# Optimization experiments

Measured on AMD Instinct MI355X. Metric: run time of the kernel, lower is better.

The kernel has to match this reference:

```python
import jax, jax.numpy as jnp
import numpy as np

B, N, D, H, V, E, T = 128, 49, 512, 512, 10000, 512, 20


def setup_inputs() -> dict:
    key = jax.random.key(0)
    ks = jax.random.split(key, 12)
    s = 0.02  # weight init scale
    return {
        "img_features": jax.random.normal(ks[0], (B, N, D), jnp.float32),
        "captions": jax.random.randint(ks[1], (B, T), 0, V, jnp.int32),
        "embed": jax.random.normal(ks[2], (V, E), jnp.float32) * s,
        "W_v": jax.random.normal(ks[3], (D, D), jnp.float32) * s,
        "W_h": jax.random.normal(ks[4], (D, H), jnp.float32) * s,
        "att_b": jnp.zeros((N,), jnp.float32),
        "W_a": jax.random.normal(ks[5], (D,), jnp.float32) * s,
        "W_ih": jax.random.normal(ks[6], (4 * H, E + D), jnp.float32) * s,
        "b_ih": jnp.zeros((4 * H,), jnp.float32),
        "W_hh": jax.random.normal(ks[7], (4 * H, H), jnp.float32) * s,
        "b_hh": jnp.zeros((4 * H,), jnp.float32),
        "W_out": jax.random.normal(ks[8], (V, H), jnp.float32) * s,
        "b_out": jnp.zeros((V,), jnp.float32),
    }


def reference(img_features, captions, embed, W_v, W_h, att_b, W_a,
              W_ih, b_ih, W_hh, b_hh, W_out, b_out):
    b, n, d = img_features.shape
    t_len = captions.shape[1]
    h_dim = W_hh.shape[1]
    emb = embed[captions]                       # [B,T,E]
    mean_ctx = img_features.mean(axis=1)        # [B,D] (context at t=0)
    fv = jnp.einsum('bnd,ed->bne', img_features, W_v)  # precomputed W_v @ feats

    def step(carry, xs):
        h, c = carry
        emb_t, t = xs                           # emb_t: [B,E]
        # additive attention (computed for all t; masked out at t=0)
        oh = h @ W_h.T                          # [B,D]
        act = jax.nn.relu(fv + oh[:, None, :] + att_b[None, :, None])
        a = jax.nn.softmax(act @ W_a, axis=1)   # [B,N]
        z = jnp.einsum('bnd,bn->bd', img_features, a)
        context = jnp.where(t == 0, mean_ctx, z)
        alpha = jnp.where(t == 0, jnp.zeros_like(a), a)
        x = jnp.concatenate([context, emb_t], axis=1)   # [B, D+E]
        gates = x @ W_ih.T + b_ih + h @ W_hh.T + b_hh   # [B, 4H]
        i, f, g, o = jnp.split(gates, 4, axis=1)
        c = jax.nn.sigmoid(f) * c + jax.nn.sigmoid(i) * jnp.tanh(g)
        h = jax.nn.sigmoid(o) * jnp.tanh(c)
        out = h @ W_out.T + b_out               # [B,V]
        return (h, c), (out, alpha)

    h0 = jnp.zeros((b, h_dim), img_features.dtype)
    c0 = jnp.zeros((b, h_dim), img_features.dtype)
    _, (preds, alphas) = jax.lax.scan(
        step, (h0, c0), (emb.transpose(1, 0, 2), jnp.arange(t_len)))
    predictions = preds.transpose(1, 0, 2)      # [B,T,V]
    alphas = alphas.transpose(1, 2, 0)          # [B,N,T]
    return predictions, alphas
```

## Files before the change

kernel.cpp:

```cpp
#include <hip/hip_runtime.h>
#include <hip/hip_bf16.h>

#define BB 128
#define NN 49
#define VV 10000
#define TT 20

typedef short s8x8 __attribute__((ext_vector_type(8)));
typedef __bf16 bf8x8 __attribute__((ext_vector_type(8)));
typedef float f32x4 __attribute__((ext_vector_type(4)));
typedef unsigned long long ull;
typedef ull ull2 __attribute__((ext_vector_type(2)));

__device__ __forceinline__ float bf2f(short s){ return (float)__builtin_bit_cast(__bf16, s); }
__device__ __forceinline__ short f2bf(float f){ return __builtin_bit_cast(short, (__bf16)f); }

__device__ __forceinline__ s8x8 cast8(const float* p){
  float4 a = *(const float4*)p;
  float4 b = *(const float4*)(p + 4);
  s8x8 r;
  r[0] = f2bf(a.x); r[1] = f2bf(a.y); r[2] = f2bf(a.z); r[3] = f2bf(a.w);
  r[4] = f2bf(b.x); r[5] = f2bf(b.y); r[6] = f2bf(b.z); r[7] = f2bf(b.w);
  return r;
}

__device__ __forceinline__ f32x4 mfma16(s8x8 a, s8x8 b, f32x4 c){
  return __builtin_amdgcn_mfma_f32_16x16x32_bf16(
      __builtin_bit_cast(bf8x8, a), __builtin_bit_cast(bf8x8, b), c, 0, 0, 0);
}

__device__ __forceinline__ ull aload8(const short* p){
  return __hip_atomic_load((const ull*)p, __ATOMIC_RELAXED, __HIP_MEMORY_SCOPE_AGENT);
}
__device__ __forceinline__ void astore8(short* p, ull v){
  __hip_atomic_store((ull*)p, v, __ATOMIC_RELAXED, __HIP_MEMORY_SCOPE_AGENT);
}

__device__ __forceinline__ void grid_bar(unsigned* bar, int inst, int nblk){
  __syncthreads();
  if (threadIdx.x == 0){
    unsigned* base = bar + inst*512;
    int g = blockIdx.x & 15;
    __hip_atomic_fetch_add(base + g*32, 1u, __ATOMIC_RELAXED, __HIP_MEMORY_SCOPE_AGENT);
    for (;;){
      unsigned s = 0;
      #pragma unroll
      for (int i = 0; i < 16; i++)
        s += __hip_atomic_load(base + i*32, __ATOMIC_RELAXED, __HIP_MEMORY_SCOPE_AGENT);
      if (s >= (unsigned)nblk) break;
      __builtin_amdgcn_s_sleep(4);
    }
  }
  __syncthreads();
}

__global__ __launch_bounds__(256) void k_prep2(
    const float* __restrict__ Whh, const float* __restrict__ Wih,
    const float* __restrict__ Wh,
    short* __restrict__ wcatp, short* __restrict__ whp)
{
  const long CW = 393216;
  const long CH = 32768;
  for (long c = blockIdx.x*256L + threadIdx.x; c < CW + CH; c += (long)gridDim.x*256L){
    if (c < CW){
      long s = c*8;
      int jt = (int)(s / 196608);
      int r  = (int)(s % 196608);
      int it = r >> 13;
      int r2 = r & 8191;
      int row = r2 >> 6, kk = r2 & 63;
      int jg = ((row>>5)<<9) + jt*32 + (row&31);
      int k = it*64 + kk;
      const float* src = (k < 512) ? (Whh + (long)jg*512 + k)
                                   : (Wih + (long)jg*1024 + (k - 512));
      *(s8x8*)(wcatp + s) = cast8(src);
    } else {
      long j = (c - CW)*8;
      *(s8x8*)(whp + j) = cast8(Wh + j);
    }
  }
}

__global__ __launch_bounds__(256) void k_packout(const float* __restrict__ Wout,
                                                 short* __restrict__ woutbf)
{
  for (long c = blockIdx.x*256L + threadIdx.x; c < 640000; c += (long)gridDim.x*256L)
    *(s8x8*)(woutbf + c*8) = cast8(Wout + c*8);
}

__global__ __launch_bounds__(256) void k_fv(const float* __restrict__ img,
    const float* __restrict__ Wv, const float* __restrict__ attb,
    short* __restrict__ fvbf)
{
  const int n0 = blockIdx.x*128, m0 = blockIdx.y*128;
  __shared__ short As[128*40];
  __shared__ short Bs[128*40];
  const int tid = threadIdx.x, w = tid>>6, lane = tid&63;
  f32x4 acc[8][2] = {};
  for (int k0 = 0; k0 < 512; k0 += 32){
    for (int c = tid; c < 512; c += 256){
      int row = c>>2, ko = (c&3)*8;
      *(s8x8*)(As + row*40 + ko) = cast8(img + (long)(m0+row)*512 + k0 + ko);
      *(s8x8*)(Bs + row*40 + ko) = cast8(Wv  + (long)(n0+row)*512 + k0 + ko);
    }
    __syncthreads();
    const int kb = (lane>>4)*8, l15 = lane&15;
    s8x8 b0f = *(const s8x8*)(Bs + (w*32 + l15)*40 + kb);
    s8x8 b1f = *(const s8x8*)(Bs + (w*32 + 16 + l15)*40 + kb);
    #pragma unroll
    for (int mt = 0; mt < 8; mt++){
      s8x8 a = *(const s8x8*)(As + (mt*16 + l15)*40 + kb);
      acc[mt][0] = mfma16(a, b0f, acc[mt][0]);
      acc[mt][1] = mfma16(a, b1f, acc[mt][1]);
    }
    __syncthreads();
  }
  const int l15 = lane&15;
  #pragma unroll
  for (int mt = 0; mt < 8; mt++){
    int rb = m0 + mt*16 + ((lane>>4)<<2);
    #pragma unroll
    for (int nt = 0; nt < 2; nt++){
      int cg = n0 + w*32 + nt*16 + l15;
      #pragma unroll
      for (int rr = 0; rr < 4; rr++){
        int r = rb + rr;
        fvbf[(long)r*512 + cg] = f2bf(acc[mt][nt][rr] + attb[r % NN]);
      }
    }
  }
}

__global__ __launch_bounds__(256) void k_loop(
    const short* __restrict__ whp, const short* __restrict__ fvbf,
    const float* __restrict__ Wa, const float* __restrict__ img,
    const short* __restrict__ wcatp, const float* __restrict__ embed,
    const int* __restrict__ caps, const float* __restrict__ bih,
    const float* __restrict__ bhh, short* __restrict__ Hbuf,
    short* __restrict__ Cbuf, float* __restrict__ cst,
    short* __restrict__ Hall, float* __restrict__ alph,
    unsigned* __restrict__ bar)
{
  __shared__ float hs[512];
  __shared__ float ohs[512];
  __shared__ float ee[64];
  __shared__ float zp[4][512];
  __shared__ short xs[16][1024];
  __shared__ short As[16*76];
  __shared__ short Bs[128*76];
  __shared__ float gs[16][132];
  __shared__ short hsb[16][32];

  const int bid = blockIdx.x, tid = threadIdx.x;
  const int w = tid>>6, lane = tid&63;

  for (int t = 0; t < TT; t++){
    const short* Hcur = Hbuf + (t&1)*65536;
    short*       Hnxt = Hbuf + ((t+1)&1)*65536;

    {
      const int b = bid;
      if (t == 0){
        for (int d = tid; d < 512; d += 256){
          float s = 0.f;
          for (int n = 0; n < NN; n++) s += img[((long)b*NN + n)*512 + d];
          zp[0][d] = s * (1.f/49.f);
        }
        __syncthreads();
        if (tid < 64){
          int dd = tid*8;
          s8x8 o;
          #pragma unroll
          for (int q = 0; q < 8; q++) o[q] = f2bf(zp[0][dd+q]);
          ull2 u = __builtin_bit_cast(ull2, o);
          astore8(Cbuf + b*512 + dd, u.x);
          astore8(Cbuf + b*512 + dd + 4, u.y);
        }
        if (tid < NN) alph[((long)b*NN + tid)*TT] = 0.f;
      } else {
        for (int i = tid; i < 128; i += 256){
          ull u = aload8(Hcur + (long)b*512 + i*4);
          short4 sv = __builtin_bit_cast(short4, u);
          hs[i*4+0] = bf2f(sv.x); hs[i*4+1] = bf2f(sv.y);
          hs[i*4+2] = bf2f(sv.z); hs[i*4+3] = bf2f(sv.w);
        }
        __syncthreads();
        for (int d = tid; d < 512; d += 256){
          const short* wr = whp + (long)d*512;
          float s = 0.f;
          for (int j8 = 0; j8 < 512; j8 += 8){
            s8x8 v = *(const s8x8*)(wr + j8);
            #pragma unroll
            for (int q = 0; q < 8; q++) s = fmaf(hs[j8+q], bf2f(v[q]), s);
          }
          ohs[d] = s;
        }
        __syncthreads();
        float ohr[8], war[8];
        {
          const float* wp = Wa + lane*8;
          #pragma unroll
          for (int q = 0; q < 8; q++){ ohr[q] = ohs[lane*8 + q]; war[q] = wp[q]; }
        }
        for (int n = w; n < NN; n += 4){
          s8x8 v = *(const s8x8*)(fvbf + ((long)b*NN + n)*512 + lane*8);
          float s = 0.f;
          #pragma unroll
          for (int q = 0; q < 8; q++)
            s = fmaf(fmaxf(bf2f(v[q]) + ohr[q], 0.f), war[q], s);
          #pragma unroll
          for (int off = 32; off; off >>= 1) s += __shfl_xor(s, off);
          if (lane == 0) ee[n] = s;
        }
        __syncthreads();
        if (tid < 64){
          float e = (tid < NN) ? ee[tid] : -1e30f;
          float m = e;
          #pragma unroll
          for (int off = 32; off; off >>= 1) m = fmaxf(m, __shfl_xor(m, off));
          float ex = (tid < NN) ? __expf(e - m) : 0.f;
          float s = ex;
          #pragma unroll
          for (int off = 32; off; off >>= 1) s += __shfl_xor(s, off);
          float a = ex / s;
          if (tid < NN){ ee[tid] = a; alph[((long)b*NN + tid)*TT + t] = a; }
        }
        __syncthreads();
        const int cq = tid>>6, d0 = (tid&63)*8;
        float z[8] = {0,0,0,0,0,0,0,0};
        for (int n = cq; n < NN; n += 4){
          float an = ee[n];
          const float* ip = img + ((long)b*NN + n)*512 + d0;
          float4 u0 = *(const float4*)ip;
          float4 u1 = *(const float4*)(ip + 4);
          z[0] = fmaf(an, u0.x, z[0]); z[1] = fmaf(an, u0.y, z[1]);
          z[2] = fmaf(an, u0.z, z[2]); z[3] = fmaf(an, u0.w, z[3]);
          z[4] = fmaf(an, u1.x, z[4]); z[5] = fmaf(an, u1.y, z[5]);
          z[6] = fmaf(an, u1.z, z[6]); z[7] = fmaf(an, u1.w, z[7]);
        }
        #pragma unroll
        for (int q = 0; q < 8; q++) zp[cq][d0 + q] = z[q];
        __syncthreads();
        if (tid < 64){
          int dd = tid*8;
          s8x8 o;
          #pragma unroll
          for (int q = 0; q < 8; q++)
            o[q] = f2bf(zp[0][dd+q] + zp[1][dd+q] + zp[2][dd+q] + zp[3][dd+q]);
          ull2 u = __builtin_bit_cast(ull2, o);
          astore8(Cbuf + b*512 + dd, u.x);
          astore8(Cbuf + b*512 + dd + 4, u.y);
        }
      }
    }
    grid_bar(bar, 2*t, 128);

    {
      const int jt = bid >> 3, b0 = (bid & 7)*16;
      const int J0 = jt*32;
      const long wbase = (long)jt*24*8192;

      for (int i = tid; i < 4096; i += 256){
        int bl = i >> 8, q = (i & 255)*4;
        ull u = 0;
        if (q < 512){
          if (t != 0) u = aload8(Hcur + (long)(b0+bl)*512 + q);
        } else {
          u = aload8(Cbuf + (long)(b0+bl)*512 + (q - 512));
        }
        *(ull*)(&xs[bl][q]) = u;
      }
      __syncthreads();

      s8x8 a_r, b_r[4];
      auto stage_load = [&](int it){
        if (tid < 128){
          int row = tid>>3, kkc = (tid&7)*8;
          int k = it*64 + kkc;
          s8x8 av;
          if (k < 1024) av = *(const s8x8*)(&xs[row][k]);
          else av = cast8(embed + (long)caps[(b0+row)*TT + t]*512 + (k - 1024));
          a_r = av;
        }
        #pragma unroll
        for (int i = 0; i < 4; i++){
          long c = tid + i*256;
          b_r[i] = *(const s8x8*)(wcatp + wbase + (long)it*8192 + c*8);
        }
      };

      f32x4 acc[2] = {};
      stage_load(0);
      for (int it = 0; it < 24; ++it){
        if (tid < 128)
          *(s8x8*)(As + (tid>>3)*76 + (tid&7)*8) = a_r;
        #pragma unroll
        for (int i = 0; i < 4; i++){
          int c = tid + i*256;
          *(s8x8*)(Bs + (c>>3)*76 + (c&7)*8) = b_r[i];
        }
        __syncthreads();
        if (it < 23) stage_load(it + 1);
        const int kb = (lane>>4)*8, l15 = lane&15, cw = w*32;
        #pragma unroll
        for (int ks = 0; ks < 2; ks++){
          s8x8 b0f = *(const s8x8*)(Bs + (cw + l15)*76 + kb + ks*32);
          s8x8 b1f = *(const s8x8*)(Bs + (cw + 16 + l15)*76 + kb + ks*32);
          s8x8 a = *(const s8x8*)(As + l15*76 + kb + ks*32);
          acc[0] = mfma16(a, b0f, acc[0]);
          acc[1] = mfma16(a, b1f, acc[1]);
        }
        __syncthreads();
      }
      {
        const int l15 = lane&15;
        int rl = (lane>>4)<<2;
        #pragma unroll
        for (int nt = 0; nt < 2; nt++){
          int ct = w*32 + nt*16 + l15;
          #pragma unroll
          for (int rr = 0; rr < 4; rr++)
            gs[rl+rr][ct] = acc[nt][rr];
        }
      }
      __syncthreads();
      for (int task = tid; task < 512; task += 256){
        int bl = task>>5, jc = task&31;
        int gb = b0 + bl, j = J0 + jc;
        float gi = gs[bl][jc]      + bih[j]        + bhh[j];
        float gf = gs[bl][32+jc]   + bih[512+j]    + bhh[512+j];
        float gg = gs[bl][64+jc]   + bih[1024+j]   + bhh[1024+j];
        float go = gs[bl][96+jc]   + bih[1536+j]   + bhh[1536+j];
        float ii = 1.f/(1.f+__expf(-gi));
        float ff = 1.f/(1.f+__expf(-gf));
        float e2 = __expf(2.f*gg); float g2 = (e2-1.f)/(e2+1.f);
        float oo = 1.f/(1.f+__expf(-go));
        float cp = (t == 0) ? 0.f : cst[gb*512 + j];
        float cN = ff*cp + ii*g2;
        float e3 = __expf(2.f*cN); float th = (e3-1.f)/(e3+1.f);
        float hN = oo*th;
        cst[gb*512 + j] = cN;
        short hb = f2bf(hN);
        hsb[bl][jc] = hb;
        Hall[((long)gb*TT + t)*512 + j] = hb;
      }
      __syncthreads();
      if (tid < 128){
        int row = tid>>3, c4 = (tid&7)*4;
        ull u = *(const ull*)(&hsb[row][c4]);
        astore8(Hnxt + (long)(b0+row)*512 + J0 + c4, u);
      }
    }
    grid_bar(bar, 2*t + 1, 128);
  }
}

__global__ __launch_bounds__(256) void k_out(const short* __restrict__ Abf,
    const short* __restrict__ Bbf, float* __restrict__ outf,
    const float* __restrict__ bias)
{
  int flat = blockIdx.y*79 + blockIdx.x;
  int xcd = flat & 7, idx = flat >> 3;
  int wg = (xcd < 4) ? xcd*198 + idx : 792 + (xcd-4)*197 + idx;
  const int n0 = (wg/20)*128, m0 = (wg%20)*128;
  __shared__ short As[128*40];
  __shared__ short Bs[128*40];
  const int tid = threadIdx.x, w = tid>>6, lane = tid&63;
  f32x4 acc[8][2] = {};
  for (int k0 = 0; k0 < 512; k0 += 32){
    for (int c = tid; c < 512; c += 256){
      int row = c>>2, ko = (c&3)*8;
      *(s8x8*)(As + row*40 + ko) = *(const s8x8*)(Abf + (long)(m0+row)*512 + k0 + ko);
      int brow = n0 + row;
      s8x8 bv = {0,0,0,0,0,0,0,0};
      if (brow < VV) bv = *(const s8x8*)(Bbf + (long)brow*512 + k0 + ko);
      *(s8x8*)(Bs + row*40 + ko) = bv;
    }
    __syncthreads();
    const int kb = (lane>>4)*8, l15 = lane&15;
    s8x8 b0f = *(const s8x8*)(Bs + (w*32 + l15)*40 + kb);
    s8x8 b1f = *(const s8x8*)(Bs + (w*32 + 16 + l15)*40 + kb);
    #pragma unroll
    for (int mt = 0; mt < 8; mt++){
      s8x8 a = *(const s8x8*)(As + (mt*16 + l15)*40 + kb);
      acc[mt][0] = mfma16(a, b0f, acc[mt][0]);
      acc[mt][1] = mfma16(a, b1f, acc[mt][1]);
    }
    __syncthreads();
  }
  const int l15 = lane&15;
  #pragma unroll
  for (int mt = 0; mt < 8; mt++){
    int rb = m0 + mt*16 + ((lane>>4)<<2);
    #pragma unroll
    for (int nt = 0; nt < 2; nt++){
      int cg = n0 + w*32 + nt*16 + l15;
      if (cg >= VV) continue;
      #pragma unroll
      for (int rr = 0; rr < 4; rr++){
        int r = rb + rr;
        outf[(long)r*VV + cg] = acc[mt][nt][rr] + bias[cg];
      }
    }
  }
}

extern "C" void kernel_launch(void* const* d_in, const int* in_sizes, int n_in,
                              void* d_out, int out_size, void* d_ws, size_t ws_size,
                              hipStream_t stream)
{
  const float* img  = (const float*)d_in[0];
  const int*   caps = (const int*)d_in[1];
  const float* emb  = (const float*)d_in[2];
  const float* Wv   = (const float*)d_in[3];
  const float* Wh   = (const float*)d_in[4];
  const float* attb = (const float*)d_in[5];
  const float* Wa   = (const float*)d_in[6];
  const float* Wih  = (const float*)d_in[7];
  const float* bih  = (const float*)d_in[8];
  const float* Whh  = (const float*)d_in[9];
  const float* bhh  = (const float*)d_in[10];
  const float* Wout = (const float*)d_in[11];
  const float* bout = (const float*)d_in[12];
  float* preds = (float*)d_out;
  float* alph  = preds + (long)BB*TT*VV;

  char* ws = (char*)d_ws;
  short* wcatp  = (short*)(ws);
  short* whp    = (short*)(ws + 6291456);
  short* fvbf   = (short*)(ws + 6815744);
  short* Hbuf   = (short*)(ws + 13238272);
  short* Cbuf   = (short*)(ws + 13500416);
  float* cst    = (float*)(ws + 13631488);
  short* Hall   = (short*)(ws + 13893632);
  unsigned* bar = (unsigned*)(ws + 16515072);
  short* woutbf = (short*)(ws);

  hipMemsetAsync(bar, 0, 81920, stream);
  k_prep2<<<1024, 256, 0, stream>>>(Whh, Wih, Wh, wcatp, whp);
  k_fv<<<dim3(4,49), 256, 0, stream>>>(img, Wv, attb, fvbf);

  k_loop<<<128, 256, 0, stream>>>(whp, fvbf, Wa, img, wcatp, emb, caps,
                                  bih, bhh, Hbuf, Cbuf, cst, Hall, alph, bar);

  k_packout<<<1024, 256, 0, stream>>>(Wout, woutbf);
  k_out<<<dim3(79,20), 256, 0, stream>>>(Hall, woutbf, preds, bout);
}
```

Baseline: 1.154 ms.

## Split persistent recurrent kernel into per-timestep launches with one grid barrier

```diff
diff --git a/kernel.cpp b/kernel.cpp
--- a/kernel.cpp
+++ b/kernel.cpp
@@ -131,7 +131,7 @@
   }
 }
 
-__global__ __launch_bounds__(256) void k_loop(
+__global__ __launch_bounds__(256) void k_step(
     const short* __restrict__ whp, const short* __restrict__ fvbf,
     const float* __restrict__ Wa, const float* __restrict__ img,
     const short* __restrict__ wcatp, const float* __restrict__ embed,
@@ -139,7 +139,7 @@
     const float* __restrict__ bhh, short* __restrict__ Hbuf,
     short* __restrict__ Cbuf, float* __restrict__ cst,
     short* __restrict__ Hall, float* __restrict__ alph,
-    unsigned* __restrict__ bar)
+    unsigned* __restrict__ bar, int t)
 {
   __shared__ float hs[512];
   __shared__ float ohs[512];
@@ -149,209 +149,211 @@
   __shared__ short As[16*76];
   __shared__ short Bs[128*76];
   __shared__ float gs[16][132];
-  __shared__ short hsb[16][32];
 
   const int bid = blockIdx.x, tid = threadIdx.x;
   const int w = tid>>6, lane = tid&63;
-
-  for (int t = 0; t < TT; t++){
-    const short* Hcur = Hbuf + (t&1)*65536;
-    short*       Hnxt = Hbuf + ((t+1)&1)*65536;
-
+  const short* Hcur = Hbuf + (t&1)*65536;
+  short*       Hnxt = Hbuf + ((t+1)&1)*65536;
+
+  {
+    const int b0g = (bid & 7)*16;
+    for (int i = tid; i < 2048; i += 256){
+      int bl = i >> 7, q = (i & 127)*4;
+      ull u = 0;
+      if (t != 0) u = *(const ull*)(Hcur + (long)(b0g+bl)*512 + q);
+      *(ull*)(&xs[bl][q]) = u;
+    }
+  }
+
+  {
+    const int b = bid;
+    if (t == 0){
+      for (int d = tid; d < 512; d += 256){
+        float s = 0.f;
+        for (int n = 0; n < NN; n++) s += img[((long)b*NN + n)*512 + d];
+        zp[0][d] = s * (1.f/49.f);
+      }
+      __syncthreads();
+      if (tid < 64){
+        int dd = tid*8;
+        s8x8 o;
+        #pragma unroll
+        for (int q = 0; q < 8; q++) o[q] = f2bf(zp[0][dd+q]);
+        ull2 u = __builtin_bit_cast(ull2, o);
+        astore8(Cbuf + b*512 + dd, u.x);
+        astore8(Cbuf + b*512 + dd + 4, u.y);
+      }
+      if (tid < NN) alph[((long)b*NN + tid)*TT] = 0.f;
+    } else {
+      for (int d = tid; d < 512; d += 256) hs[d] = bf2f(Hcur[b*512 + d]);
+      __syncthreads();
+      for (int d = tid; d < 512; d += 256){
+        const short* wr = whp + (long)d*512;
+        float s = 0.f;
+        for (int j8 = 0; j8 < 512; j8 += 8){
+          s8x8 v = *(const s8x8*)(wr + j8);
+          #pragma unroll
+          for (int q = 0; q < 8; q++) s = fmaf(hs[j8+q], bf2f(v[q]), s);
+        }
+        ohs[d] = s;
+      }
+      __syncthreads();
+      float ohr[8], war[8];
+      {
+        const float* wp = Wa + lane*8;
+        #pragma unroll
+        for (int q = 0; q < 8; q++){ ohr[q] = ohs[lane*8 + q]; war[q] = wp[q]; }
+      }
+      for (int n = w; n < NN; n += 4){
+        s8x8 v = *(const s8x8*)(fvbf + ((long)b*NN + n)*512 + lane*8);
+        float s = 0.f;
+        #pragma unroll
+        for (int q = 0; q < 8; q++)
+          s = fmaf(fmaxf(bf2f(v[q]) + ohr[q], 0.f), war[q], s);
+        #pragma unroll
+        for (int off = 32; off; off >>= 1) s += __shfl_xor(s, off);
+        if (lane == 0) ee[n] = s;
+      }
+      __syncthreads();
+      if (tid < 64){
+        float e = (tid < NN) ? ee[tid] : -1e30f;
+        float m = e;
+        #pragma unroll
+        for (int off = 32; off; off >>= 1) m = fmaxf(m, __shfl_xor(m, off));
+        float ex = (tid < NN) ? __expf(e - m) : 0.f;
+        float s = ex;
+        #pragma unroll
+        for (int off = 32; off; off >>= 1) s += __shfl_xor(s, off);
+        float a = ex / s;
+        if (tid < NN){ ee[tid] = a; alph[((long)b*NN + tid)*TT + t] = a; }
+      }
+      __syncthreads();
+      const int cq = tid>>6, d0 = (tid&63)*8;
+      float z[8] = {0,0,0,0,0,0,0,0};
+      for (int n = cq; n < NN; n += 4){
+        float an = ee[n];
+        const float* ip = img + ((long)b*NN + n)*512 + d0;
+        float4 u0 = *(const float4*)ip;
+        float4 u1 = *(const float4*)(ip + 4);
+        z[0] = fmaf(an, u0.x, z[0]); z[1] = fmaf(an, u0.y, z[1]);
+        z[2] = fmaf(an, u0.z, z[2]); z[3] = fmaf(an, u0.w, z[3]);
+        z[4] = fmaf(an, u1.x, z[4]); z[5] = fmaf(an, u1.y, z[5]);
+        z[6] = fmaf(an, u1.z, z[6]); z[7] = fmaf(an, u1.w, z[7]);
+      }
+      #pragma unroll
+      for (int q = 0; q < 8; q++) zp[cq][d0 + q] = z[q];
+      __syncthreads();
+      if (tid < 64){
+        int dd = tid*8;
+        s8x8 o;
+        #pragma unroll
+        for (int q = 0; q < 8; q++)
+          o[q] = f2bf(zp[0][dd+q] + zp[1][dd+q] + zp[2][dd+q] + zp[3][dd+q]);
+        ull2 u = __builtin_bit_cast(ull2, o);
+        astore8(Cbuf + b*512 + dd, u.x);
+        astore8(Cbuf + b*512 + dd + 4, u.y);
+      }
+    }
+  }
+  grid_bar(bar, t, 128);
+
+  {
+    const int jt = bid >> 3, b0 = (bid & 7)*16;
+    const int J0 = jt*32;
+    const long wbase = (long)jt*24*8192;
+
+    for (int i = tid; i < 2048; i += 256){
+      int bl = i >> 7, q = (i & 127)*4;
+      ull u = aload8(Cbuf + (long)(b0+bl)*512 + q);
+      *(ull*)(&xs[bl][512 + q]) = u;
+    }
+    __syncthreads();
+
+    auto lda = [&](int it) -> s8x8 {
+      s8x8 av = {0,0,0,0,0,0,0,0};
+      if (tid < 128){
+        int row = tid>>3, kkc = (tid&7)*8;
+        int k = it*64 + kkc;
+        if (k < 1024) av = *(const s8x8*)(&xs[row][k]);
+        else av = cast8(embed + (long)caps[(b0+row)*TT + t]*512 + (k - 1024));
+      }
+      return av;
+    };
+    auto ldb = [&](int it, s8x8* br){
+      #pragma unroll
+      for (int i = 0; i < 4; i++){
+        long c = tid + i*256;
+        br[i] = *(const s8x8*)(wcatp + wbase + (long)it*8192 + c*8);
+      }
+    };
+    auto put = [&](s8x8 av, const s8x8* br){
+      if (tid < 128)
+        *(s8x8*)(As + (tid>>3)*76 + (tid&7)*8) = av;
+      #pragma unroll
+      for (int i = 0; i < 4; i++){
+        int c = tid + i*256;
+        *(s8x8*)(Bs + (c>>3)*76 + (c&7)*8) = br[i];
+      }
+    };
+
+    f32x4 acc[2] = {};
+    const int kb = (lane>>4)*8, l15 = lane&15, cw = w*32;
+    auto mmas = [&](){
+      #pragma unroll
+      for (int ks = 0; ks < 2; ks++){
+        s8x8 b0f = *(const s8x8*)(Bs + (cw + l15)*76 + kb + ks*32);
+        s8x8 b1f = *(const s8x8*)(Bs + (cw + 16 + l15)*76 + kb + ks*32);
+        s8x8 a = *(const s8x8*)(As + l15*76 + kb + ks*32);
+        acc[0] = mfma16(a, b0f, acc[0]);
+        acc[1] = mfma16(a, b1f, acc[1]);
+      }
+    };
+
+    s8x8 a0 = lda(0), a1 = lda(1), b0r[4], b1r[4];
+    ldb(0, b0r); ldb(1, b1r);
+    for (int it2 = 0; it2 < 24; it2 += 2){
+      put(a0, b0r);
+      __syncthreads();
+      if (it2 + 2 < 24){ a0 = lda(it2+2); ldb(it2+2, b0r); }
+      mmas();
+      __syncthreads();
+      put(a1, b1r);
+      __syncthreads();
+      if (it2 + 3 < 24){ a1 = lda(it2+3); ldb(it2+3, b1r); }
+      mmas();
+      __syncthreads();
+    }
     {
-      const int b = bid;
-      if (t == 0){
-        for (int d = tid; d < 512; d += 256){
-          float s = 0.f;
-          for (int n = 0; n < NN; n++) s += img[((long)b*NN + n)*512 + d];
-          zp[0][d] = s * (1.f/49.f);
-        }
-        __syncthreads();
-        if (tid < 64){
-          int dd = tid*8;
-          s8x8 o;
-          #pragma unroll
-          for (int q = 0; q < 8; q++) o[q] = f2bf(zp[0][dd+q]);
-          ull2 u = __builtin_bit_cast(ull2, o);
-          astore8(Cbuf + b*512 + dd, u.x);
-          astore8(Cbuf + b*512 + dd + 4, u.y);
-        }
-        if (tid < NN) alph[((long)b*NN + tid)*TT] = 0.f;
-      } else {
-        for (int i = tid; i < 128; i += 256){
-          ull u = aload8(Hcur + (long)b*512 + i*4);
-          short4 sv = __builtin_bit_cast(short4, u);
-          hs[i*4+0] = bf2f(sv.x); hs[i*4+1] = bf2f(sv.y);
-          hs[i*4+2] = bf2f(sv.z); hs[i*4+3] = bf2f(sv.w);
-        }
-        __syncthreads();
-        for (int d = tid; d < 512; d += 256){
-          const short* wr = whp + (long)d*512;
-          float s = 0.f;
-          for (int j8 = 0; j8 < 512; j8 += 8){
-            s8x8 v = *(const s8x8*)(wr + j8);
-            #pragma unroll
-            for (int q = 0; q < 8; q++) s = fmaf(hs[j8+q], bf2f(v[q]), s);
-          }
-          ohs[d] = s;
-        }
-        __syncthreads();
-        float ohr[8], war[8];
-        {
-          const float* wp = Wa + lane*8;
-          #pragma unroll
-          for (int q = 0; q < 8; q++){ ohr[q] = ohs[lane*8 + q]; war[q] = wp[q]; }
-        }
-        for (int n = w; n < NN; n += 4){
-          s8x8 v = *(const s8x8*)(fvbf + ((long)b*NN + n)*512 + lane*8);
-          float s = 0.f;
-          #pragma unroll
-          for (int q = 0; q < 8; q++)
-            s = fmaf(fmaxf(bf2f(v[q]) + ohr[q], 0.f), war[q], s);
-          #pragma unroll
-          for (int off = 32; off; off >>= 1) s += __shfl_xor(s, off);
-          if (lane == 0) ee[n] = s;
-        }
-        __syncthreads();
-        if (tid < 64){
-          float e = (tid < NN) ? ee[tid] : -1e30f;
-          float m = e;
-          #pragma unroll
-          for (int off = 32; off; off >>= 1) m = fmaxf(m, __shfl_xor(m, off));
-          float ex = (tid < NN) ? __expf(e - m) : 0.f;
-          float s = ex;
-          #pragma unroll
-          for (int off = 32; off; off >>= 1) s += __shfl_xor(s, off);
-          float a = ex / s;
-          if (tid < NN){ ee[tid] = a; alph[((long)b*NN + tid)*TT + t] = a; }
-        }
-        __syncthreads();
-        const int cq = tid>>6, d0 = (tid&63)*8;
-        float z[8] = {0,0,0,0,0,0,0,0};
-        for (int n = cq; n < NN; n += 4){
-          float an = ee[n];
-          const float* ip = img + ((long)b*NN + n)*512 + d0;
-          float4 u0 = *(const float4*)ip;
-          float4 u1 = *(const float4*)(ip + 4);
-          z[0] = fmaf(an, u0.x, z[0]); z[1] = fmaf(an, u0.y, z[1]);
-          z[2] = fmaf(an, u0.z, z[2]); z[3] = fmaf(an, u0.w, z[3]);
-          z[4] = fmaf(an, u1.x, z[4]); z[5] = fmaf(an, u1.y, z[5]);
-          z[6] = fmaf(an, u1.z, z[6]); z[7] = fmaf(an, u1.w, z[7]);
-        }
-        #pragma unroll
-        for (int q = 0; q < 8; q++) zp[cq][d0 + q] = z[q];
-        __syncthreads();
-        if (tid < 64){
-          int dd = tid*8;
-          s8x8 o;
-          #pragma unroll
-          for (int q = 0; q < 8; q++)
-            o[q] = f2bf(zp[0][dd+q] + zp[1][dd+q] + zp[2][dd+q] + zp[3][dd+q]);
-          ull2 u = __builtin_bit_cast(ull2, o);
-          astore8(Cbuf + b*512 + dd, u.x);
-          astore8(Cbuf + b*512 + dd + 4, u.y);
-        }
-      }
-    }
-    grid_bar(bar, 2*t, 128);
-
-    {
-      const int jt = bid >> 3, b0 = (bid & 7)*16;
-      const int J0 = jt*32;
-      const long wbase = (long)jt*24*8192;
-
-      for (int i = tid; i < 4096; i += 256){
-        int bl = i >> 8, q = (i & 255)*4;
-        ull u = 0;
-        if (q < 512){
-          if (t != 0) u = aload8(Hcur + (long)(b0+bl)*512 + q);
-        } else {
-          u = aload8(Cbuf + (long)(b0+bl)*512 + (q - 512));
-        }
-        *(ull*)(&xs[bl][q]) = u;
-      }
-      __syncthreads();
-
-      s8x8 a_r, b_r[4];
-      auto stage_load = [&](int it){
-        if (tid < 128){
-          int row = tid>>3, kkc = (tid&7)*8;
-          int k = it*64 + kkc;
-          s8x8 av;
-          if (k < 1024) av = *(const s8x8*)(&xs[row][k]);
-          else av = cast8(embed + (long)caps[(b0+row)*TT + t]*512 + (k - 1024));
-          a_r = av;
-        }
-        #pragma unroll
-        for (int i = 0; i < 4; i++){
-          long c = tid + i*256;
-          b_r[i] = *(const s8x8*)(wcatp + wbase + (long)it*8192 + c*8);
-        }
-      };
-
-      f32x4 acc[2] = {};
-      stage_load(0);
-      for (int it = 0; it < 24; ++it){
-        if (tid < 128)
-          *(s8x8*)(As + (tid>>3)*76 + (tid&7)*8) = a_r;
-        #pragma unroll
-        for (int i = 0; i < 4; i++){
-          int c = tid + i*256;
-          *(s8x8*)(Bs + (c>>3)*76 + (c&7)*8) = b_r[i];
-        }
-        __syncthreads();
-        if (it < 23) stage_load(it + 1);
-        const int kb = (lane>>4)*8, l15 = lane&15, cw = w*32;
-        #pragma unroll
-        for (int ks = 0; ks < 2; ks++){
-          s8x8 b0f = *(const s8x8*)(Bs + (cw + l15)*76 + kb + ks*32);
-          s8x8 b1f = *(const s8x8*)(Bs + (cw + 16 + l15)*76 + kb + ks*32);
-          s8x8 a = *(const s8x8*)(As + l15*76 + kb + ks*32);
-          acc[0] = mfma16(a, b0f, acc[0]);
-          acc[1] = mfma16(a, b1f, acc[1]);
-        }
-        __syncthreads();
-      }
-      {
-        const int l15 = lane&15;
-        int rl = (lane>>4)<<2;
-        #pragma unroll
-        for (int nt = 0; nt < 2; nt++){
-          int ct = w*32 + nt*16 + l15;
-          #pragma unroll
-          for (int rr = 0; rr < 4; rr++)
-            gs[rl+rr][ct] = acc[nt][rr];
-        }
-      }
-      __syncthreads();
-      for (int task = tid; task < 512; task += 256){
-        int bl = task>>5, jc = task&31;
-        int gb = b0 + bl, j = J0 + jc;
-        float gi = gs[bl][jc]      + bih[j]        + bhh[j];
-        float gf = gs[bl][32+jc]   + bih[512+j]    + bhh[512+j];
-        float gg = gs[bl][64+jc]   + bih[1024+j]   + bhh[1024+j];
-        float go = gs[bl][96+jc]   + bih[1536+j]   + bhh[1536+j];
-        float ii = 1.f/(1.f+__expf(-gi));
-        float ff = 1.f/(1.f+__expf(-gf));
-        float e2 = __expf(2.f*gg); float g2 = (e2-1.f)/(e2+1.f);
-        float oo = 1.f/(1.f+__expf(-go));
-        float cp = (t == 0) ? 0.f : cst[gb*512 + j];
-        float cN = ff*cp + ii*g2;
-        float e3 = __expf(2.f*cN); float th = (e3-1.f)/(e3+1.f);
-        float hN = oo*th;
-        cst[gb*512 + j] = cN;
-        short hb = f2bf(hN);
-        hsb[bl][jc] = hb;
-        Hall[((long)gb*TT + t)*512 + j] = hb;
-      }
-      __syncthreads();
-      if (tid < 128){
-        int row = tid>>3, c4 = (tid&7)*4;
-        ull u = *(const ull*)(&hsb[row][c4]);
-        astore8(Hnxt + (long)(b0+row)*512 + J0 + c4, u);
-      }
-    }
-    grid_bar(bar, 2*t + 1, 128);
+      int rl = (lane>>4)<<2;
+      #pragma unroll
+      for (int nt = 0; nt < 2; nt++){
+        int ct = cw + nt*16 + l15;
+        #pragma unroll
+        for (int rr = 0; rr < 4; rr++)
+          gs[rl+rr][ct] = acc[nt][rr];
+      }
+    }
+    __syncthreads();
+    for (int task = tid; task < 512; task += 256){
+      int bl = task>>5, jc = task&31;
+      int gb = b0 + bl, j = J0 + jc;
+      float gi = gs[bl][jc]      + bih[j]        + bhh[j];
+      float gf = gs[bl][32+jc]   + bih[512+j]    + bhh[512+j];
+      float gg = gs[bl][64+jc]   + bih[1024+j]   + bhh[1024+j];
+      float go = gs[bl][96+jc]   + bih[1536+j]   + bhh[1536+j];
+      float ii = 1.f/(1.f+__expf(-gi));
+      float ff = 1.f/(1.f+__expf(-gf));
+      float e2 = __expf(2.f*gg); float g2 = (e2-1.f)/(e2+1.f);
+      float oo = 1.f/(1.f+__expf(-go));
+      float cp = (t == 0) ? 0.f : cst[gb*512 + j];
+      float cN = ff*cp + ii*g2;
+      float e3 = __expf(2.f*cN); float th = (e3-1.f)/(e3+1.f);
+      float hN = oo*th;
+      cst[gb*512 + j] = cN;
+      short hb = f2bf(hN);
+      Hnxt[gb*512 + j] = hb;
+      Hall[((long)gb*TT + t)*512 + j] = hb;
+    }
   }
 }
 
@@ -440,8 +442,10 @@
   k_prep2<<<1024, 256, 0, stream>>>(Whh, Wih, Wh, wcatp, whp);
   k_fv<<<dim3(4,49), 256, 0, stream>>>(img, Wv, attb, fvbf);
 
-  k_loop<<<128, 256, 0, stream>>>(whp, fvbf, Wa, img, wcatp, emb, caps,
-                                  bih, bhh, Hbuf, Cbuf, cst, Hall, alph, bar);
+  for (int t = 0; t < TT; t++)
+    k_step<<<128, 256, 0, stream>>>(whp, fvbf, Wa, img, wcatp, emb, caps,
+                                    bih, bhh, Hbuf, Cbuf, cst, Hall, alph,
+                                    bar, t);
 
   k_packout<<<1024, 256, 0, stream>>>(Wout, woutbf);
   k_out<<<dim3(79,20), 256, 0, stream>>>(Hall, woutbf, preds, bout);
```

Result: faster. 1.016 ms (-12.0%).
